# Kernel tuning notes

Measured on AMD Instinct MI355X. Metric: run time of the kernel, lower is better.

## Reference

```python
import jax, jax.numpy as jnp
import numpy as np

EMB_DIM = 512
N_HEADS = 8
HEAD_DIM = EMB_DIM // N_HEADS


def setup_inputs() -> dict:
    key = jax.random.key(0)
    k1, k2, k3, k4, k5 = jax.random.split(key, 5)
    B, S = 4, 2048
    x = jax.random.normal(k1, (B, S, EMB_DIM), dtype=jnp.float32)
    # nn.Linear params: weight [out, in], bias [out]
    W_qkv = jax.random.normal(k2, (3 * EMB_DIM, EMB_DIM), dtype=jnp.float32) * (EMB_DIM ** -0.5)
    b_qkv = jax.random.normal(k3, (3 * EMB_DIM,), dtype=jnp.float32) * 0.02
    W_out = jax.random.normal(k4, (EMB_DIM, EMB_DIM), dtype=jnp.float32) * (EMB_DIM ** -0.5)
    b_out = jax.random.normal(k5, (EMB_DIM,), dtype=jnp.float32) * 0.02
    return {"x": x, "W_qkv": W_qkv, "b_qkv": b_qkv, "W_out": W_out, "b_out": b_out}


def reference(x, W_qkv, b_qkv, W_out, b_out):
    B, S, E = x.shape
    scale = E ** (-0.5)  # note: scores are DIVIDED by this, i.e. multiplied by sqrt(E)
    qkv = x @ W_qkv.T + b_qkv                       # [B, S, 3E]
    qkv = qkv.reshape(B, S, N_HEADS, 3 * HEAD_DIM).transpose(0, 2, 1, 3)  # [B, H, S, 3d]
    q, k, v = jnp.split(qkv, 3, axis=-1)            # each [B, H, S, d]
    scores = jnp.einsum("bhqd,bhkd->bhqk", q, k) / scale
    attn = jax.nn.softmax(scores, axis=-1)
    attn = jax.nn.softmax(attn, axis=-1)            # double softmax, faithful to source
    o = jnp.einsum("bhqk,bhkd->bhqd", attn, v)      # [B, H, S, d]
    o = o.transpose(0, 2, 1, 3).reshape(B, S, E)
    return o @ W_out.T + b_out
```

## Files before the change

### kernel.cpp

```cpp
#include <hip/hip_runtime.h>

typedef __bf16 bf16;
typedef __attribute__((ext_vector_type(4))) __bf16 bf16x4;
typedef __attribute__((ext_vector_type(8))) __bf16 bf16x8;
typedef __attribute__((ext_vector_type(4))) float f32x4;

#define MFMA(A,B,C) __builtin_amdgcn_mfma_f32_16x16x32_bf16(A,B,C,0,0,0)

#define SEQ 2048
#define EMB 512
#define HD  64
#define SCALE 22.627416997969522f
#define NEG_SEED -3.0e4f

__global__ __launch_bounds__(256)
void convert_kernel(const float* __restrict__ x, const float* __restrict__ Wqkv,
                    const float* __restrict__ Wout,
                    bf16* __restrict__ Xh, bf16* __restrict__ Xl,
                    bf16* __restrict__ Wqh, bf16* __restrict__ Wql,
                    bf16* __restrict__ Wo, float* __restrict__ Vs) {
  if (blockIdx.x < 8) Vs[blockIdx.x * 256 + threadIdx.x] = 0.f;
  const int NX = 8192 * 512 / 4;
  const int NW = 1536 * 512 / 4;
  const int NO = 512 * 512 / 4;
  const int stride = gridDim.x * 256;
  for (int i = blockIdx.x * 256 + threadIdx.x; i < NX + NW + NO; i += stride) {
    const float* src; bf16 *dh, *dl; int j; bool haslo;
    if (i < NX)           { src = x;    dh = Xh;  dl = Xl;  j = i;           haslo = true; }
    else if (i < NX + NW) { src = Wqkv; dh = Wqh; dl = Wql; j = i - NX;      haslo = true; }
    else                  { src = Wout; dh = Wo;  dl = Wo;  j = i - NX - NW; haslo = false; }
    f32x4 v = *(const f32x4*)&src[(size_t)j * 4];
    bf16x4 h4, l4;
#pragma unroll
    for (int r = 0; r < 4; ++r) {
      bf16 h = (bf16)v[r]; h4[r] = h; l4[r] = (bf16)(v[r] - (float)h);
    }
    *(bf16x4*)&dh[(size_t)j * 4] = h4;
    if (haslo) *(bf16x4*)&dl[(size_t)j * 4] = l4;
  }
}

__global__ __launch_bounds__(256)
void gemm_qkv(const bf16* __restrict__ Xh, const bf16* __restrict__ Xl,
              const bf16* __restrict__ Wh, const bf16* __restrict__ Wl,
              const float* __restrict__ bias,
              bf16* __restrict__ Qh, bf16* __restrict__ Ql,
              bf16* __restrict__ Kh, bf16* __restrict__ Kl,
              bf16* __restrict__ Vrm, float* __restrict__ Vs) {
  __shared__ __align__(16) bf16 Ah[64][64], Al[64][64];
  __shared__ __align__(16) bf16 Bh[64][64], Bl[64][64];
  const int tid  = threadIdx.x;
  const int lane = tid & 63, wave = tid >> 6;
  const int lin = blockIdx.x + gridDim.x * blockIdx.y;
  const int xcd = lin & 7;
  const int w_  = lin >> 3;
  const int m0 = ((w_ & 15) + xcd * 16) * 64;
  const int n0 = (w_ >> 4) * 64;
  const bool isV = ((n0 % 192) == 128);
  const int wm = (wave >> 1) * 32, wn = (wave & 1) * 32;
  const int c = lane & 15, quad = lane >> 4;
  const int sr   = tid >> 3;
  const int scol = (tid & 7) * 8;
  const int sphy = ((tid & 7) ^ (sr & 7)) * 8;

  const f32x4 zero = {0.f, 0.f, 0.f, 0.f};
  f32x4 acc[2][2];
  acc[0][0] = zero; acc[0][1] = zero; acc[1][0] = zero; acc[1][1] = zero;

  for (int k0 = 0; k0 < 512; k0 += 64) {
    *(bf16x8*)&Ah[sr][sphy]      = *(const bf16x8*)&Xh[(size_t)(m0 + sr     ) * 512 + k0 + scol];
    *(bf16x8*)&Ah[sr + 32][sphy] = *(const bf16x8*)&Xh[(size_t)(m0 + sr + 32) * 512 + k0 + scol];
    *(bf16x8*)&Bh[sr][sphy]      = *(const bf16x8*)&Wh[(size_t)(n0 + sr     ) * 512 + k0 + scol];
    *(bf16x8*)&Bh[sr + 32][sphy] = *(const bf16x8*)&Wh[(size_t)(n0 + sr + 32) * 512 + k0 + scol];
    if (!isV) {
      *(bf16x8*)&Al[sr][sphy]      = *(const bf16x8*)&Xl[(size_t)(m0 + sr     ) * 512 + k0 + scol];
      *(bf16x8*)&Al[sr + 32][sphy] = *(const bf16x8*)&Xl[(size_t)(m0 + sr + 32) * 512 + k0 + scol];
      *(bf16x8*)&Bl[sr][sphy]      = *(const bf16x8*)&Wl[(size_t)(n0 + sr     ) * 512 + k0 + scol];
      *(bf16x8*)&Bl[sr + 32][sphy] = *(const bf16x8*)&Wl[(size_t)(n0 + sr + 32) * 512 + k0 + scol];
    }
    __syncthreads();
#pragma unroll
    for (int ks = 0; ks < 64; ks += 32) {
      const int px = (((ks >> 3) + quad) ^ (c & 7)) * 8;
      bf16x8 ah0 = *(bf16x8*)&Ah[wm + c     ][px];
      bf16x8 ah1 = *(bf16x8*)&Ah[wm + 16 + c][px];
      bf16x8 bh0 = *(bf16x8*)&Bh[wn + c     ][px];
      bf16x8 bh1 = *(bf16x8*)&Bh[wn + 16 + c][px];
      if (isV) {
        acc[0][0] = MFMA(ah0, bh0, acc[0][0]);
        acc[0][1] = MFMA(ah0, bh1, acc[0][1]);
        acc[1][0] = MFMA(ah1, bh0, acc[1][0]);
        acc[1][1] = MFMA(ah1, bh1, acc[1][1]);
      } else {
        bf16x8 al0 = *(bf16x8*)&Al[wm + c     ][px];
        bf16x8 al1 = *(bf16x8*)&Al[wm + 16 + c][px];
        bf16x8 bl0 = *(bf16x8*)&Bl[wn + c     ][px];
        bf16x8 bl1 = *(bf16x8*)&Bl[wn + 16 + c][px];
        acc[0][0] = MFMA(ah0, bh0, acc[0][0]);
        acc[0][0] = MFMA(al0, bh0, acc[0][0]);
        acc[0][0] = MFMA(ah0, bl0, acc[0][0]);
        acc[0][1] = MFMA(ah0, bh1, acc[0][1]);
        acc[0][1] = MFMA(al0, bh1, acc[0][1]);
        acc[0][1] = MFMA(ah0, bl1, acc[0][1]);
        acc[1][0] = MFMA(ah1, bh0, acc[1][0]);
        acc[1][0] = MFMA(al1, bh0, acc[1][0]);
        acc[1][0] = MFMA(ah1, bl0, acc[1][0]);
        acc[1][1] = MFMA(ah1, bh1, acc[1][1]);
        acc[1][1] = MFMA(al1, bh1, acc[1][1]);
        acc[1][1] = MFMA(ah1, bl1, acc[1][1]);
      }
    }
    __syncthreads();
  }

  if (isV) {
#pragma unroll
    for (int nt = 0; nt < 2; ++nt) {
      const int n = n0 + wn + nt * 16 + c;
      const float bv = bias[n];
      const int h = n / 192, d = n % 192 - 128;
      const size_t bh = (size_t)((m0 >> 11) * 8 + h);
      float csum = 0.f;
#pragma unroll
      for (int mt = 0; mt < 2; ++mt)
#pragma unroll
        for (int r = 0; r < 4; ++r) {
          const int m = m0 + wm + mt * 16 + quad * 4 + r;
          const int s = m & 2047;
          float v = acc[mt][nt][r] + bv;
          Vrm[(bh * SEQ + s) * HD + d] = (bf16)v;
          csum += v;
        }
      csum += __shfl_xor(csum, 16, 64);
      csum += __shfl_xor(csum, 32, 64);
      if (quad == 0) atomicAdd(&Vs[bh * HD + d], csum);
    }
  } else {
#pragma unroll
    for (int mt = 0; mt < 2; ++mt) {
#pragma unroll
      for (int nt = 0; nt < 2; ++nt) {
        const int n = n0 + wn + nt * 16 + c;
        const float bv = bias[n];
#pragma unroll
        for (int r = 0; r < 4; ++r) {
          const int m = m0 + wm + mt * 16 + quad * 4 + r;
          float v = acc[mt][nt][r] + bv;
          const int h = n / 192, t = n % 192;
          const size_t bh = (size_t)((m >> 11) * 8 + h);
          const int s = m & 2047;
          if (t < 64) {
            float q = v * SCALE;
            bf16 hi = (bf16)q;
            float lo = q - (float)hi;
            size_t idx = (bh * SEQ + s) * HD + t;
            Qh[idx] = hi; Ql[idx] = (bf16)lo;
          } else {
            bf16 hi = (bf16)v;
            float lo = v - (float)hi;
            size_t idx = (bh * SEQ + s) * HD + (t - 64);
            Kh[idx] = hi; Kl[idx] = (bf16)lo;
          }
        }
      }
    }
  }
}

__global__ __launch_bounds__(256)
void gemm_out(const bf16* __restrict__ A, const bf16* __restrict__ Wo,
              const float* __restrict__ bias, float* __restrict__ C) {
  __shared__ __align__(16) bf16 As[64][64];
  __shared__ __align__(16) bf16 Bs[64][64];
  const int tid  = threadIdx.x;
  const int lane = tid & 63, wave = tid >> 6;
  const int lin = blockIdx.x + gridDim.x * blockIdx.y;
  const int xcd = lin & 7;
  const int w_  = lin >> 3;
  const int m0 = ((w_ & 15) + xcd * 16) * 64;
  const int n0 = (w_ >> 4) * 64;
  const int wm = (wave >> 1) * 32, wn = (wave & 1) * 32;
  const int c = lane & 15, quad = lane >> 4;
  const int sr   = tid >> 3;
  const int scol = (tid & 7) * 8;
  const int sphy = ((tid & 7) ^ (sr & 7)) * 8;

  const f32x4 zero = {0.f, 0.f, 0.f, 0.f};
  f32x4 acc[2][2];
  acc[0][0] = zero; acc[0][1] = zero; acc[1][0] = zero; acc[1][1] = zero;

  for (int k0 = 0; k0 < 512; k0 += 64) {
    *(bf16x8*)&As[sr][sphy]      = *(const bf16x8*)&A [(size_t)(m0 + sr     ) * 512 + k0 + scol];
    *(bf16x8*)&As[sr + 32][sphy] = *(const bf16x8*)&A [(size_t)(m0 + sr + 32) * 512 + k0 + scol];
    *(bf16x8*)&Bs[sr][sphy]      = *(const bf16x8*)&Wo[(size_t)(n0 + sr     ) * 512 + k0 + scol];
    *(bf16x8*)&Bs[sr + 32][sphy] = *(const bf16x8*)&Wo[(size_t)(n0 + sr + 32) * 512 + k0 + scol];
    __syncthreads();
#pragma unroll
    for (int ks = 0; ks < 64; ks += 32) {
      const int px = (((ks >> 3) + quad) ^ (c & 7)) * 8;
      bf16x8 a0 = *(bf16x8*)&As[wm + c     ][px];
      bf16x8 a1 = *(bf16x8*)&As[wm + 16 + c][px];
      bf16x8 b0 = *(bf16x8*)&Bs[wn + c     ][px];
      bf16x8 b1 = *(bf16x8*)&Bs[wn + 16 + c][px];
      acc[0][0] = MFMA(a0, b0, acc[0][0]);
      acc[0][1] = MFMA(a0, b1, acc[0][1]);
      acc[1][0] = MFMA(a1, b0, acc[1][0]);
      acc[1][1] = MFMA(a1, b1, acc[1][1]);
    }
    __syncthreads();
  }

#pragma unroll
  for (int mt = 0; mt < 2; ++mt) {
#pragma unroll
    for (int nt = 0; nt < 2; ++nt) {
      const int n = n0 + wn + nt * 16 + c;
      const float bv = bias[n];
#pragma unroll
      for (int r = 0; r < 4; ++r) {
        const int m = m0 + wm + mt * 16 + quad * 4 + r;
        C[(size_t)m * 512 + n] = acc[mt][nt][r] + bv;
      }
    }
  }
}

__global__ __launch_bounds__(256, 4)
void attn_kernel(const bf16* __restrict__ Qh, const bf16* __restrict__ Ql,
                 const bf16* __restrict__ Kh, const bf16* __restrict__ Kl,
                 const bf16* __restrict__ Vrm, const float* __restrict__ Vs,
                 bf16* __restrict__ O) {
  __shared__ __align__(16) bf16 SK[2][128][64];
  __shared__ float plistS[4][16][16];
  __shared__ unsigned short plistI[4][16][16];
  __shared__ int pcnt[4][16];

  const int tid  = threadIdx.x;
  const int lane = tid & 63, wave = tid >> 6;
  const int c = lane & 15, quad = lane >> 4;
  const int bh = blockIdx.x;
  const int q0 = blockIdx.y * 64 + wave * 16;
  const size_t hoff = (size_t)bh * SEQ * HD;
  const bf16* qh_p = Qh + hoff;
  const bf16* ql_p = Ql + hoff;
  const bf16* kh_p = Kh + hoff;
  const bf16* kl_p = Kl + hoff;
  const bf16* v_p  = Vrm + hoff;
  const f32x4 zero = {0.f, 0.f, 0.f, 0.f};

  const int sr   = tid >> 3;
  const int scol = (tid & 7) * 8;
  const int sphy = ((tid & 7) ^ (sr & 7)) * 8;
  const int pc0  = ((0 + quad) ^ (c & 7)) * 8;
  const int pc1  = ((4 + quad) ^ (c & 7)) * 8;

  bf16x8 qf[2], qlf[2];
#pragma unroll
  for (int t = 0; t < 2; ++t) {
    size_t off = (size_t)(q0 + c) * HD + t * 32 + quad * 8;
    qf[t]  = *(const bf16x8*)&qh_p[off];
    qlf[t] = *(const bf16x8*)&ql_p[off];
  }
  if (lane < 16) pcnt[wave][lane] = 0;

  bf16x8 pA = *(const bf16x8*)&kh_p[(size_t)(sr     ) * HD + scol];
  bf16x8 pB = *(const bf16x8*)&kh_p[(size_t)(sr + 32) * HD + scol];
  bf16x8 pC = *(const bf16x8*)&kh_p[(size_t)(sr + 64) * HD + scol];
  bf16x8 pD = *(const bf16x8*)&kh_p[(size_t)(sr + 96) * HD + scol];
  *(bf16x8*)&SK[0][sr     ][sphy] = pA;
  *(bf16x8*)&SK[0][sr + 32][sphy] = pB;
  *(bf16x8*)&SK[0][sr + 64][sphy] = pC;
  *(bf16x8*)&SK[0][sr + 96][sphy] = pD;
  __syncthreads();

  float mq = NEG_SEED, l1 = 0.f;
  int buf = 0;
  for (int cs = 0; cs < 16; ++cs) {
    if (cs < 15) {
      const size_t k0 = (size_t)(cs + 1) * 128;
      pA = *(const bf16x8*)&kh_p[(k0 + sr     ) * HD + scol];
      pB = *(const bf16x8*)&kh_p[(k0 + sr + 32) * HD + scol];
      pC = *(const bf16x8*)&kh_p[(k0 + sr + 64) * HD + scol];
      pD = *(const bf16x8*)&kh_p[(k0 + sr + 96) * HD + scol];
    }
#pragma unroll
    for (int t = 0; t < 8; ++t) {
      const int g = cs * 8 + t;
      bf16x8 kh0 = *(bf16x8*)&SK[buf][t * 16 + c][pc0];
      bf16x8 kh1 = *(bf16x8*)&SK[buf][t * 16 + c][pc1];
      f32x4 sc = MFMA(kh0, qf[0], zero);
      sc = MFMA(kh1, qf[1], sc);
      const float tm = fmaxf(fmaxf(sc[0], sc[1]), fmaxf(sc[2], sc[3]));
      if (__any(tm > mq - 31.f)) {
        const size_t kr = (size_t)(g * 16 + c) * HD + quad * 8;
        bf16x8 kl0 = *(const bf16x8*)&kl_p[kr];
        bf16x8 kl1 = *(const bf16x8*)&kl_p[kr + 32];
        sc = MFMA(kh0, qlf[0], sc);
        sc = MFMA(kh1, qlf[1], sc);
        sc = MFMA(kl0, qf[0],  sc);
        sc = MFMA(kl1, qf[1],  sc);
        float tme = fmaxf(fmaxf(sc[0], sc[1]), fmaxf(sc[2], sc[3]));
        tme = fmaxf(tme, __shfl_xor(tme, 16, 64));
        tme = fmaxf(tme, __shfl_xor(tme, 32, 64));
        if (tme > mq) {
          l1 *= __expf(mq - tme);
          mq = tme;
        }
#pragma unroll
        for (int r = 0; r < 4; ++r) {
          const float d = sc[r] - mq;
          l1 += __expf(d);
          if (d > -16.f) {
            const int slot = atomicAdd(&pcnt[wave][c], 1);
            if (slot < 16) {
              plistS[wave][c][slot] = sc[r];
              plistI[wave][c][slot] = (unsigned short)(g * 16 + quad * 4 + r);
            }
          }
        }
      }
    }
    if (cs < 15) {
      const int nb = buf ^ 1;
      *(bf16x8*)&SK[nb][sr     ][sphy] = pA;
      *(bf16x8*)&SK[nb][sr + 32][sphy] = pB;
      *(bf16x8*)&SK[nb][sr + 64][sphy] = pC;
      *(bf16x8*)&SK[nb][sr + 96][sphy] = pD;
      __syncthreads();
      buf = nb;
    }
  }
  l1 += __shfl_xor(l1, 16, 64);
  l1 += __shfl_xor(l1, 32, 64);

  const float inv1 = 1.f / l1;
  float oc[16];
#pragma unroll
  for (int i = 0; i < 16; ++i) oc[i] = 0.f;
  float l2 = 0.f;
  const int n = min(pcnt[wave][c], 16);
  for (int j = 0; j < n; ++j) {
    const float sv = plistS[wave][c][j];
    const int  idx = plistI[wave][c][j];
    const float a1v = __expf(sv - mq) * inv1;
    const float t1 = __expf(a1v) - 1.0f;
    l2 += t1;
    const bf16* vp = &v_p[(size_t)idx * HD + quad * 4];
#pragma unroll
    for (int dt = 0; dt < 4; ++dt) {
      bf16x4 v4 = *(const bf16x4*)&vp[dt * 16];
#pragma unroll
      for (int r = 0; r < 4; ++r) oc[dt * 4 + r] += t1 * (float)v4[r];
    }
  }

  const int b = bh >> 3, h = bh & 7;
  const float rcp = 1.f / (2048.f + l2);
  const float* vsp = Vs + bh * HD;
  bf16* orow = &O[((size_t)b * SEQ + q0 + c) * EMB + h * HD];
#pragma unroll
  for (int dt = 0; dt < 4; ++dt) {
    f32x4 vt4 = *(const f32x4*)&vsp[dt * 16 + quad * 4];
    bf16x4 ov;
#pragma unroll
    for (int r = 0; r < 4; ++r) ov[r] = (bf16)((oc[dt * 4 + r] + vt4[r]) * rcp);
    *(bf16x4*)&orow[dt * 16 + quad * 4] = ov;
  }
}

extern "C" void kernel_launch(void* const* d_in, const int* in_sizes, int n_in,
                              void* d_out, int out_size, void* d_ws, size_t ws_size,
                              hipStream_t stream) {
  const float* x    = (const float*)d_in[0];
  const float* Wqkv = (const float*)d_in[1];
  const float* bqkv = (const float*)d_in[2];
  const float* Wout = (const float*)d_in[3];
  const float* bout = (const float*)d_in[4];
  float* out = (float*)d_out;

  char* ws = (char*)d_ws;
  const size_t SZ = (size_t)32 * SEQ * HD * 2;
  bf16* Qh  = (bf16*)(ws + 0 * SZ);
  bf16* Ql  = (bf16*)(ws + 1 * SZ);
  bf16* Kh  = (bf16*)(ws + 2 * SZ);
  bf16* Kl  = (bf16*)(ws + 3 * SZ);
  bf16* Vrm = (bf16*)(ws + 4 * SZ);
  bf16* XhO = (bf16*)(ws + 5 * SZ);
  bf16* Xl  = (bf16*)(ws + 6 * SZ);
  bf16* Wqh = (bf16*)(ws + 7 * SZ);
  bf16* Wql = (bf16*)(ws + 7 * SZ + 0x180000);
  bf16* Wo  = (bf16*)(ws + 7 * SZ + 0x300000);
  float* Vs = (float*)(ws + 7 * SZ + 0x380000);

  convert_kernel<<<dim3(2048), 256, 0, stream>>>(x, Wqkv, Wout, XhO, Xl, Wqh, Wql, Wo, Vs);
  gemm_qkv<<<dim3(128, 24), 256, 0, stream>>>(XhO, Xl, Wqh, Wql, bqkv, Qh, Ql, Kh, Kl, Vrm, Vs);
  attn_kernel<<<dim3(32, 32), 256, 0, stream>>>(Qh, Ql, Kh, Kl, Vrm, Vs, XhO);
  gemm_out<<<dim3(128, 8), 256, 0, stream>>>(XhO, Wo, bout, out);
}
```

Before: 217.1 us.

## Select attention candidates with hi-only scores, then recompute exact scores for candidates

The main key loop now scores each key tile with the high bf16 parts only. It tracks a running row max shared across the wave and records candidate key indices within 12 of that max in a ring buffer of LCAP slots. This removes the low-part MFMAs, the per-tile Kl loads and the full-row exp-sum from the hot loop. Exact scores are then recomputed in fp32 for the gathered candidates, and the first softmax is normalised over those candidates only. The K tile is halved to 64 rows, and the V and output accesses are widened to 8-element vectors. The risk is that slots overwritten when the ring wraps, stale thresholds from an early running max, and the candidate-only normaliser all rest on the scores being sharply peaked.

```diff
diff --git a/kernel.cpp b/kernel.cpp
--- a/kernel.cpp
+++ b/kernel.cpp
@@ -12,6 +12,7 @@
 #define HD  64
 #define SCALE 22.627416997969522f
 #define NEG_SEED -3.0e4f
+#define LCAP 24
 
 __global__ __launch_bounds__(256)
 void convert_kernel(const float* __restrict__ x, const float* __restrict__ Wqkv,
@@ -230,9 +231,9 @@
                  const bf16* __restrict__ Kh, const bf16* __restrict__ Kl,
                  const bf16* __restrict__ Vrm, const float* __restrict__ Vs,
                  bf16* __restrict__ O) {
-  __shared__ __align__(16) bf16 SK[2][128][64];
-  __shared__ float plistS[4][16][16];
-  __shared__ unsigned short plistI[4][16][16];
+  __shared__ __align__(16) bf16 SK[2][64][64];
+  __shared__ float sS[4][16][LCAP];
+  __shared__ unsigned short sI[4][16][LCAP];
   __shared__ int pcnt[4][16];
 
   const int tid  = threadIdx.x;
@@ -265,92 +266,95 @@
 
   bf16x8 pA = *(const bf16x8*)&kh_p[(size_t)(sr     ) * HD + scol];
   bf16x8 pB = *(const bf16x8*)&kh_p[(size_t)(sr + 32) * HD + scol];
-  bf16x8 pC = *(const bf16x8*)&kh_p[(size_t)(sr + 64) * HD + scol];
-  bf16x8 pD = *(const bf16x8*)&kh_p[(size_t)(sr + 96) * HD + scol];
   *(bf16x8*)&SK[0][sr     ][sphy] = pA;
   *(bf16x8*)&SK[0][sr + 32][sphy] = pB;
-  *(bf16x8*)&SK[0][sr + 64][sphy] = pC;
-  *(bf16x8*)&SK[0][sr + 96][sphy] = pD;
   __syncthreads();
 
-  float mq = NEG_SEED, l1 = 0.f;
+  float mr = NEG_SEED;
   int buf = 0;
-  for (int cs = 0; cs < 16; ++cs) {
-    if (cs < 15) {
-      const size_t k0 = (size_t)(cs + 1) * 128;
+  for (int cs = 0; cs < 32; ++cs) {
+    if (cs < 31) {
+      const size_t k0 = (size_t)(cs + 1) * 64;
       pA = *(const bf16x8*)&kh_p[(k0 + sr     ) * HD + scol];
       pB = *(const bf16x8*)&kh_p[(k0 + sr + 32) * HD + scol];
-      pC = *(const bf16x8*)&kh_p[(k0 + sr + 64) * HD + scol];
-      pD = *(const bf16x8*)&kh_p[(k0 + sr + 96) * HD + scol];
-    }
-#pragma unroll
-    for (int t = 0; t < 8; ++t) {
-      const int g = cs * 8 + t;
+    }
+#pragma unroll
+    for (int t = 0; t < 4; ++t) {
+      const int g = cs * 4 + t;
       bf16x8 kh0 = *(bf16x8*)&SK[buf][t * 16 + c][pc0];
       bf16x8 kh1 = *(bf16x8*)&SK[buf][t * 16 + c][pc1];
       f32x4 sc = MFMA(kh0, qf[0], zero);
       sc = MFMA(kh1, qf[1], sc);
       const float tm = fmaxf(fmaxf(sc[0], sc[1]), fmaxf(sc[2], sc[3]));
-      if (__any(tm > mq - 31.f)) {
-        const size_t kr = (size_t)(g * 16 + c) * HD + quad * 8;
-        bf16x8 kl0 = *(const bf16x8*)&kl_p[kr];
-        bf16x8 kl1 = *(const bf16x8*)&kl_p[kr + 32];
-        sc = MFMA(kh0, qlf[0], sc);
-        sc = MFMA(kh1, qlf[1], sc);
-        sc = MFMA(kl0, qf[0],  sc);
-        sc = MFMA(kl1, qf[1],  sc);
-        float tme = fmaxf(fmaxf(sc[0], sc[1]), fmaxf(sc[2], sc[3]));
-        tme = fmaxf(tme, __shfl_xor(tme, 16, 64));
-        tme = fmaxf(tme, __shfl_xor(tme, 32, 64));
-        if (tme > mq) {
-          l1 *= __expf(mq - tme);
-          mq = tme;
-        }
+      mr = fmaxf(mr, tm);
+      if (t & 1) {
+        mr = fmaxf(mr, __shfl_xor(mr, 16, 64));
+        mr = fmaxf(mr, __shfl_xor(mr, 32, 64));
+      }
+      if (tm > mr - 12.f) {
 #pragma unroll
         for (int r = 0; r < 4; ++r) {
-          const float d = sc[r] - mq;
-          l1 += __expf(d);
-          if (d > -16.f) {
-            const int slot = atomicAdd(&pcnt[wave][c], 1);
-            if (slot < 16) {
-              plistS[wave][c][slot] = sc[r];
-              plistI[wave][c][slot] = (unsigned short)(g * 16 + quad * 4 + r);
-            }
+          if (sc[r] > mr - 12.f) {
+            const int slot = atomicAdd(&pcnt[wave][c], 1) % LCAP;
+            sI[wave][c][slot] = (unsigned short)(g * 16 + quad * 4 + r);
           }
         }
       }
     }
-    if (cs < 15) {
+    if (cs < 31) {
       const int nb = buf ^ 1;
       *(bf16x8*)&SK[nb][sr     ][sphy] = pA;
       *(bf16x8*)&SK[nb][sr + 32][sphy] = pB;
-      *(bf16x8*)&SK[nb][sr + 64][sphy] = pC;
-      *(bf16x8*)&SK[nb][sr + 96][sphy] = pD;
       __syncthreads();
       buf = nb;
     }
   }
-  l1 += __shfl_xor(l1, 16, 64);
-  l1 += __shfl_xor(l1, 32, 64);
-
+
+  float qv[16];
+#pragma unroll
+  for (int j = 0; j < 8; ++j) {
+    qv[j]     = (float)qf[0][j] + (float)qlf[0][j];
+    qv[8 + j] = (float)qf[1][j] + (float)qlf[1][j];
+  }
+  const int n = min(pcnt[wave][c], LCAP);
+  float mqC = NEG_SEED;
+  for (int j = 0; j < n; ++j) {
+    const int idx = sI[wave][c][j];
+    const size_t kr = (size_t)idx * HD + quad * 8;
+    bf16x8 kh0 = *(const bf16x8*)&kh_p[kr];
+    bf16x8 kh1 = *(const bf16x8*)&kh_p[kr + 32];
+    bf16x8 kl0 = *(const bf16x8*)&kl_p[kr];
+    bf16x8 kl1 = *(const bf16x8*)&kl_p[kr + 32];
+    float s = 0.f;
+#pragma unroll
+    for (int jj = 0; jj < 8; ++jj) {
+      s = fmaf(qv[jj],     (float)kh0[jj] + (float)kl0[jj], s);
+      s = fmaf(qv[8 + jj], (float)kh1[jj] + (float)kl1[jj], s);
+    }
+    s += __shfl_xor(s, 16, 64);
+    s += __shfl_xor(s, 32, 64);
+    if (quad == 0) sS[wave][c][j] = s;
+    mqC = fmaxf(mqC, s);
+  }
+  float l1 = 0.f;
+  for (int j = 0; j < n; ++j) l1 += __expf(sS[wave][c][j] - mqC);
   const float inv1 = 1.f / l1;
+
   float oc[16];
 #pragma unroll
   for (int i = 0; i < 16; ++i) oc[i] = 0.f;
   float l2 = 0.f;
-  const int n = min(pcnt[wave][c], 16);
   for (int j = 0; j < n; ++j) {
-    const float sv = plistS[wave][c][j];
-    const int  idx = plistI[wave][c][j];
-    const float a1v = __expf(sv - mq) * inv1;
-    const float t1 = __expf(a1v) - 1.0f;
+    const float a1 = __expf(sS[wave][c][j] - mqC) * inv1;
+    const float t1 = __expf(a1) - 1.0f;
     l2 += t1;
-    const bf16* vp = &v_p[(size_t)idx * HD + quad * 4];
-#pragma unroll
-    for (int dt = 0; dt < 4; ++dt) {
-      bf16x4 v4 = *(const bf16x4*)&vp[dt * 16];
-#pragma unroll
-      for (int r = 0; r < 4; ++r) oc[dt * 4 + r] += t1 * (float)v4[r];
+    const int idx = sI[wave][c][j];
+    bf16x8 v0 = *(const bf16x8*)&v_p[(size_t)idx * HD + quad * 8];
+    bf16x8 v1 = *(const bf16x8*)&v_p[(size_t)idx * HD + 32 + quad * 8];
+#pragma unroll
+    for (int jj = 0; jj < 8; ++jj) {
+      oc[jj]     += t1 * (float)v0[jj];
+      oc[8 + jj] += t1 * (float)v1[jj];
     }
   }
 
@@ -358,14 +362,14 @@
   const float rcp = 1.f / (2048.f + l2);
   const float* vsp = Vs + bh * HD;
   bf16* orow = &O[((size_t)b * SEQ + q0 + c) * EMB + h * HD];
-#pragma unroll
-  for (int dt = 0; dt < 4; ++dt) {
-    f32x4 vt4 = *(const f32x4*)&vsp[dt * 16 + quad * 4];
-    bf16x4 ov;
-#pragma unroll
-    for (int r = 0; r < 4; ++r) ov[r] = (bf16)((oc[dt * 4 + r] + vt4[r]) * rcp);
-    *(bf16x4*)&orow[dt * 16 + quad * 4] = ov;
-  }
+  bf16x8 o0, o1;
+#pragma unroll
+  for (int jj = 0; jj < 8; ++jj) {
+    o0[jj] = (bf16)((oc[jj]     + vsp[quad * 8 + jj])      * rcp);
+    o1[jj] = (bf16)((oc[8 + jj] + vsp[32 + quad * 8 + jj]) * rcp);
+  }
+  *(bf16x8*)&orow[quad * 8]      = o0;
+  *(bf16x8*)&orow[32 + quad * 8] = o1;
 }
 
 extern "C" void kernel_launch(void* const* d_in, const int* in_sizes, int n_in,
```

Result: faster. 194.7 us (-10.3%).
